# Performance work log

Measured on AMD Instinct MI355X. Metric: run time of the kernel, lower is better.

Reference implementation:

```python
import jax, jax.numpy as jnp
import numpy as np
from jax import lax

N = 100000   # input points
M = 100000   # output points
CIN = 64
COUT = 64
K = 3        # cubic kernel size
G = 50       # grid side (points live at voxel centers of a G^3 grid)
SHIFT = 1    # coordinate shift so border queries (coord -1) stay non-negative
B = 64       # per-axis encode base, > G + K; key fits easily in int32


def _encode(c):
    # c: [..., 3] int32 xyz voxel coords -> unique int32 key
    c = c + SHIFT
    return (c[..., 2] * B + c[..., 1]) * B + c[..., 0]


def setup_inputs() -> dict:
    rng = np.random.RandomState(0)
    total = G ** 3

    def decode(idx):
        x = idx % G
        y = (idx // G) % G
        z = idx // (G * G)
        # +0.5 moves points to voxel centers (as in the layer's docstring example)
        return np.stack([x, y, z], axis=1).astype(np.float32) + 0.5

    inp_positions = jnp.asarray(decode(rng.permutation(total)[:N]))
    out_positions = jnp.asarray(decode(rng.permutation(total)[:M]))

    key = jax.random.key(0)
    k1, k2 = jax.random.split(key, 2)
    inp_features = jax.random.normal(k1, (N, CIN), jnp.float32)
    kernel = jax.random.normal(k2, (K, K, K, CIN, COUT), jnp.float32) * 0.05
    bias = jnp.zeros((COUT,), jnp.float32)
    voxel_size = jnp.ones((), jnp.float32)
    return {
        "inp_features": inp_features,
        "inp_positions": inp_positions,
        "out_positions": out_positions,
        "voxel_size": voxel_size,
        "kernel": kernel,
        "bias": bias,
    }


def reference(inp_features, inp_positions, out_positions, voxel_size, kernel, bias):
    # SparseConv on a regular grid: odd cubic kernel -> offset = 0, Linf radius
    # K*voxel*0.51 selects exactly the K^3 voxel neighborhood. Nearest-neighbor
    # interpolation with identity mapping maps relative offset d in [-r, r]^3
    # to filter tap index d + r on each axis (x = width = last spatial dim).
    inp_coord = jnp.floor(inp_positions / voxel_size).astype(jnp.int32)  # [N,3]
    out_coord = jnp.floor(out_positions / voxel_size).astype(jnp.int32)  # [M,3]

    # sorted-key hash table over input voxels
    keys = _encode(inp_coord)                    # [N]
    order = jnp.argsort(keys)
    skeys = keys[order]
    feats = inp_features[order]                  # [N, Cin]

    r = K // 2
    K3 = K ** 3
    ks = jnp.arange(K3)
    # flat kernel order is (z, y, x) to match kernel.reshape(K3, Cin, Cout)
    d_xyz = jnp.stack([ks % K - r, (ks // K) % K - r, ks // (K * K) - r],
                      axis=1).astype(jnp.int32)  # [K3, 3]
    Kmat = kernel.reshape(K3, CIN, COUT)

    n_inp = skeys.shape[0]

    def step(acc, xs):
        d, W = xs                                 # d: [3], W: [Cin, Cout]
        qk = _encode(out_coord + d)               # [M]
        p = jnp.searchsorted(skeys, qk)
        pc = jnp.clip(p, 0, n_inp - 1)
        found = (skeys[pc] == qk)[:, None]        # [M, 1]
        g = jnp.where(found, feats[pc], 0.0)      # [M, Cin]
        return acc + g @ W, None

    out0 = jnp.zeros((out_coord.shape[0], COUT), inp_features.dtype)
    out, _ = lax.scan(step, out0, (d_xyz, Kmat))
    return out + bias
```

## Files before the change

### kernel.cpp

```cpp
#include <hip/hip_runtime.h>
#include <math.h>

#define GY 54
#define ZD 58
#define NROWS (ZD*GY*64)

#define HX 10
#define HY 6
#define HXY 60
#define NH 600
#define NBX 7
#define NBY 13
#define NBZ 7
#define NBRICK (NBX*NBY*NBZ)
#define SLAB 80

#define TAPS_C0 14
#define TAPS_C1 13

typedef __bf16  bf16x8 __attribute__((ext_vector_type(8)));
typedef float  f32x16 __attribute__((ext_vector_type(16)));

__global__ void prep_kernel(const float* __restrict__ ipos, int n,
                            const float* __restrict__ opos, int m,
                            const float* __restrict__ vsp,
                            const float* __restrict__ W,
                            int* __restrict__ imap, int* __restrict__ ikey,
                            int* __restrict__ omap, int* __restrict__ okey,
                            __bf16* __restrict__ Wt4) {
    int i = blockIdx.x * 256 + threadIdx.x;
    float vs = vsp[0];
    if (i < n) {
        int x = (int)floorf(ipos[3*i+0] / vs) + 1;
        int y = (int)floorf(ipos[3*i+1] / vs) + 1;
        int z = (int)floorf(ipos[3*i+2] / vs) + 1;
        int key = (z * GY + y) * 64 + x;
        ikey[i] = key;
        imap[key] = i;
    } else if (i < n + m) {
        int j = i - n;
        int x = (int)floorf(opos[3*j+0] / vs) + 1;
        int y = (int)floorf(opos[3*j+1] / vs) + 1;
        int z = (int)floorf(opos[3*j+2] / vs) + 1;
        int key = (z * GY + y) * 64 + x;
        okey[j] = key;
        omap[key] = j;
    } else if (i < n + m + 27*64*64) {
        int k  = i - n - m;
        int t  = k >> 12;
        int r  = k & 4095;
        int ci = r >> 6;
        int co = r & 63;
        int p   = ci >> 4;
        int cil = ci & 15;
        Wt4[(((p * 27 + t) << 6) + co) * 16 + cil] = (__bf16)W[k];
    }
}

#define TAP_BODY(t, tc)                                                       \
    {                                                                         \
        const int dx = (t) % 3 - 1;                                           \
        const int dy = ((t) / 3) % 3 - 1;                                     \
        const int dz = (t) / 9 - 1;                                           \
        const int doff = (dz * HXY + dy * HX + dx) * 16;                      \
        bf16x8 a0 = *(const bf16x8*)(Ab0 + doff);                             \
        bf16x8 a1 = *(const bf16x8*)(Ab1 + doff);                             \
        bf16x8 b0 = *(const bf16x8*)(Bb0 + (tc) * 1024);                      \
        bf16x8 b1 = *(const bf16x8*)(Bb1 + (tc) * 1024);                      \
        acc00 = __builtin_amdgcn_mfma_f32_32x32x16_bf16(a0, b0, acc00, 0, 0, 0); \
        acc01 = __builtin_amdgcn_mfma_f32_32x32x16_bf16(a0, b1, acc01, 0, 0, 0); \
        acc10 = __builtin_amdgcn_mfma_f32_32x32x16_bf16(a1, b0, acc10, 0, 0, 0); \
        acc11 = __builtin_amdgcn_mfma_f32_32x32x16_bf16(a1, b1, acc11, 0, 0, 0); \
    }

__global__ __launch_bounds__(256, 2) void conv_kernel(
    const float* __restrict__ feats,
    const __bf16* __restrict__ Wt4,
    const float* __restrict__ bias,
    const int*   __restrict__ imap,
    const int*   __restrict__ ikey,
    const int*   __restrict__ omap,
    const int*   __restrict__ okey,
    float*       __restrict__ out,
    int N, int M)
{
    __shared__ __align__(16) __bf16 halo[NH * 16];
    __shared__ __align__(16) __bf16 Bq[TAPS_C0 * 64 * 16];
    __shared__ int ridx[NH];
    __shared__ int obuf[256];

    const int tid = threadIdx.x;

    int q = (blockIdx.x & 7) * SLAB + (blockIdx.x >> 3);
    if (q >= NBRICK) return;
    const int bx = q % NBX;
    int rem = q / NBX;
    const int by = rem % NBY;
    const int bz = rem / NBY;

    #pragma unroll
    for (int it = 0; it < 3; ++it) {
        int r = it * 256 + tid;
        if (r < NH) {
            int xs = r % HX;
            int t2 = r / HX;
            int ys = t2 % HY;
            int zs = t2 / HY;
            int key = ((bz*8 + zs) * GY + (by*4 + ys)) * 64 + (bx*8 + xs);
            int idx = imap[key];
            int c = min(max(idx, 0), N - 1);
            ridx[r] = (idx >= 0 && idx < N && ikey[c] == key) ? idx : -1;
        }
    }
    {
        int x = tid & 7, y = (tid >> 3) & 3, z = tid >> 5;
        int key = ((bz*8 + z + 1) * GY + (by*4 + y + 1)) * 64 + (bx*8 + x + 1);
        int o = omap[key];
        int c = min(max(o, 0), M - 1);
        obuf[tid] = (o >= 0 && o < M && okey[c] == key) ? o : -1;
    }

    const int wave  = tid >> 6;
    const int lane  = tid & 63;
    const int lrow  = lane & 31;
    const int halfk = lane >> 5;
    const int xv = lrow & 7, yv = (lrow >> 3) & 3;
    const int arow0 = (2*wave + 1) * HXY + (yv + 1) * HX + (xv + 1);
    const __bf16* Ab0 = halo + arow0 * 16 + halfk * 8;
    const __bf16* Ab1 = Ab0 + HXY * 16;
    const __bf16* Bb0 = Bq + lrow * 16 + halfk * 8;
    const __bf16* Bb1 = Bb0 + 32 * 16;

    f32x16 acc00, acc01, acc10, acc11;
    #pragma unroll
    for (int i = 0; i < 16; ++i) { acc00[i]=0.f; acc01[i]=0.f; acc10[i]=0.f; acc11[i]=0.f; }

    __syncthreads();

    #pragma unroll 1
    for (int p = 0; p < 4; ++p) {
        if (p) __syncthreads();

        #pragma unroll
        for (int it = 0; it < 5; ++it) {
            int task = it * 256 + tid;
            if (task < NH * 2) {
                int r = task >> 1, hf = task & 1;
                int idx = ridx[r];
                bf16x8 v;
                if (idx >= 0) {
                    const float4* s = (const float4*)(feats + (size_t)idx * 64 + p * 16 + hf * 8);
                    float4 f0 = s[0], f1 = s[1];
                    v[0]=(__bf16)f0.x; v[1]=(__bf16)f0.y; v[2]=(__bf16)f0.z; v[3]=(__bf16)f0.w;
                    v[4]=(__bf16)f1.x; v[5]=(__bf16)f1.y; v[6]=(__bf16)f1.z; v[7]=(__bf16)f1.w;
                } else {
                    #pragma unroll
                    for (int j = 0; j < 8; ++j) v[j] = (__bf16)0.f;
                }
                *(bf16x8*)(halo + r * 16 + hf * 8) = v;
            }
        }

        {
            const __bf16* Wp = Wt4 + (size_t)p * 27648;
            #pragma unroll
            for (int it = 0; it < 7; ++it) {
                int task = it * 256 + tid;
                *(bf16x8*)(Bq + task * 8) = *(const bf16x8*)(Wp + task * 8);
            }
        }

        __syncthreads();

        #pragma unroll
        for (int t = 0; t < TAPS_C0; ++t) TAP_BODY(t, t)

        __syncthreads();

        {
            const __bf16* Wp = Wt4 + (size_t)p * 27648 + TAPS_C0 * 1024;
            #pragma unroll
            for (int it = 0; it < 7; ++it) {
                int task = it * 256 + tid;
                if (task < TAPS_C1 * 128)
                    *(bf16x8*)(Bq + task * 8) = *(const bf16x8*)(Wp + task * 8);
            }
        }

        __syncthreads();

        #pragma unroll
        for (int t = TAPS_C0; t < 27; ++t) TAP_BODY(t, t - TAPS_C0)
    }

    const int col0 = lrow, col1 = 32 + lrow;
    const float bv0 = bias[col0], bv1 = bias[col1];
    #pragma unroll
    for (int r = 0; r < 16; ++r) {
        int mrow = (r & 3) + 8 * (r >> 2) + 4 * halfk;
        int o0 = obuf[(2*wave)     * 32 + mrow];
        int o1 = obuf[(2*wave + 1) * 32 + mrow];
        if (o0 >= 0) {
            out[(size_t)o0 * 64 + col0] = acc00[r] + bv0;
            out[(size_t)o0 * 64 + col1] = acc01[r] + bv1;
        }
        if (o1 >= 0) {
            out[(size_t)o1 * 64 + col0] = acc10[r] + bv0;
            out[(size_t)o1 * 64 + col1] = acc11[r] + bv1;
        }
    }
}

extern "C" void kernel_launch(void* const* d_in, const int* in_sizes, int n_in,
                              void* d_out, int out_size, void* d_ws, size_t ws_size,
                              hipStream_t stream) {
    const float* feats = (const float*)d_in[0];
    const float* ipos  = (const float*)d_in[1];
    const float* opos  = (const float*)d_in[2];
    const float* vsp   = (const float*)d_in[3];
    const float* W     = (const float*)d_in[4];
    const float* bias  = (const float*)d_in[5];

    int N = in_sizes[0] / 64;
    int M = out_size / 64;

    int*    imap = (int*)d_ws;
    int*    omap = imap + NROWS;
    int*    ikey = omap + NROWS;
    int*    okey = ikey + N;
    __bf16* Wt4  = (__bf16*)(okey + M);

    int total = N + M + 27*64*64;
    prep_kernel<<<(total + 255) / 256, 256, 0, stream>>>(ipos, N, opos, M, vsp, W,
                                                         imap, ikey, omap, okey, Wt4);
    conv_kernel<<<8 * SLAB, 256, 0, stream>>>(feats, Wt4, bias, imap, ikey, omap, okey,
                                              (float*)d_out, N, M);
}
```

Measured before the change: 164.3 us.

## Pre-convert features to bf16 and load halo/weights via direct global-to-LDS loads

The prep kernel now converts the input features to a bf16 copy and writes a small zero row. The conv kernel then fills the halo and weight tiles with global_load_lds instead of staging them through registers, using the zero row for empty voxels. The halo halves are XOR-swizzled so MFMA operand reads avoid LDS bank conflicts, and launch bounds go from 2 to 3 blocks per CU. The cost is an extra full pass over the features in the prep kernel plus more workspace, in exchange for lower register pressure and fewer load and convert instructions in the main kernel.

```diff
diff --git a/kernel.cpp b/kernel.cpp
--- a/kernel.cpp
+++ b/kernel.cpp
@@ -18,16 +18,26 @@
 #define TAPS_C0 14
 #define TAPS_C1 13
 
+#define K3CC (27*64*64)
+
 typedef __bf16  bf16x8 __attribute__((ext_vector_type(8)));
 typedef float  f32x16 __attribute__((ext_vector_type(16)));
+
+#define AS1 __attribute__((address_space(1)))
+#define AS3 __attribute__((address_space(3)))
+#define GLD_LDS16(g, l) \
+    __builtin_amdgcn_global_load_lds((const AS1 void*)(g), (AS3 void*)(l), 16, 0, 0)
 
 __global__ void prep_kernel(const float* __restrict__ ipos, int n,
                             const float* __restrict__ opos, int m,
                             const float* __restrict__ vsp,
                             const float* __restrict__ W,
+                            const float* __restrict__ feats,
                             int* __restrict__ imap, int* __restrict__ ikey,
                             int* __restrict__ omap, int* __restrict__ okey,
-                            __bf16* __restrict__ Wt4) {
+                            __bf16* __restrict__ Wt4,
+                            __bf16* __restrict__ zrow,
+                            __bf16* __restrict__ featsB) {
     int i = blockIdx.x * 256 + threadIdx.x;
     float vs = vsp[0];
     if (i < n) {
@@ -45,7 +55,7 @@
         int key = (z * GY + y) * 64 + x;
         okey[j] = key;
         omap[key] = j;
-    } else if (i < n + m + 27*64*64) {
+    } else if (i < n + m + K3CC) {
         int k  = i - n - m;
         int t  = k >> 12;
         int r  = k & 4095;
@@ -54,28 +64,43 @@
         int p   = ci >> 4;
         int cil = ci & 15;
         Wt4[(((p * 27 + t) << 6) + co) * 16 + cil] = (__bf16)W[k];
+    } else if (i < n + m + K3CC + 32) {
+        zrow[i - n - m - K3CC] = (__bf16)0.f;
+    } else {
+        int j = i - n - m - K3CC - 32;
+        if (j < n * 8) {
+            const float4* s = (const float4*)(feats + (size_t)j * 8);
+            float4 f0 = s[0], f1 = s[1];
+            bf16x8 v;
+            v[0]=(__bf16)f0.x; v[1]=(__bf16)f0.y; v[2]=(__bf16)f0.z; v[3]=(__bf16)f0.w;
+            v[4]=(__bf16)f1.x; v[5]=(__bf16)f1.y; v[6]=(__bf16)f1.z; v[7]=(__bf16)f1.w;
+            *(bf16x8*)(featsB + (size_t)j * 8) = v;
+        }
     }
 }
 
-#define TAP_BODY(t, tc)                                                       \
-    {                                                                         \
-        const int dx = (t) % 3 - 1;                                           \
-        const int dy = ((t) / 3) % 3 - 1;                                     \
-        const int dz = (t) / 9 - 1;                                           \
-        const int doff = (dz * HXY + dy * HX + dx) * 16;                      \
-        bf16x8 a0 = *(const bf16x8*)(Ab0 + doff);                             \
-        bf16x8 a1 = *(const bf16x8*)(Ab1 + doff);                             \
-        bf16x8 b0 = *(const bf16x8*)(Bb0 + (tc) * 1024);                      \
-        bf16x8 b1 = *(const bf16x8*)(Bb1 + (tc) * 1024);                      \
+#define TAP_BODY(t, tc)                                                        \
+    {                                                                          \
+        const int drow = ((t)/9 - 1)*HXY + (((t)/3)%3 - 1)*HX + ((t)%3 - 1);   \
+        int rb  = abase + drow * 32;                                           \
+        int ad0 = rb + (((rb >> 3) & 16) ^ hk16);                              \
+        int rb1 = rb + HXY * 32;                                               \
+        int ad1 = rb1 + (((rb1 >> 3) & 16) ^ hk16);                            \
+        bf16x8 a0 = *(const bf16x8*)(haloc + ad0);                             \
+        bf16x8 a1 = *(const bf16x8*)(haloc + ad1);                             \
+        bf16x8 b0 = *(const bf16x8*)(Bb0 + (tc) * 1024);                       \
+        bf16x8 b1 = *(const bf16x8*)(Bb1 + (tc) * 1024);                       \
         acc00 = __builtin_amdgcn_mfma_f32_32x32x16_bf16(a0, b0, acc00, 0, 0, 0); \
         acc01 = __builtin_amdgcn_mfma_f32_32x32x16_bf16(a0, b1, acc01, 0, 0, 0); \
         acc10 = __builtin_amdgcn_mfma_f32_32x32x16_bf16(a1, b0, acc10, 0, 0, 0); \
         acc11 = __builtin_amdgcn_mfma_f32_32x32x16_bf16(a1, b1, acc11, 0, 0, 0); \
     }
 
-__global__ __launch_bounds__(256, 2) void conv_kernel(
+__global__ __launch_bounds__(256, 3) void conv_kernel(
     const float* __restrict__ feats,
+    const __bf16* __restrict__ featsB,
     const __bf16* __restrict__ Wt4,
+    const __bf16* __restrict__ zrow,
     const float* __restrict__ bias,
     const int*   __restrict__ imap,
     const int*   __restrict__ ikey,
@@ -126,8 +151,9 @@
     const int halfk = lane >> 5;
     const int xv = lrow & 7, yv = (lrow >> 3) & 3;
     const int arow0 = (2*wave + 1) * HXY + (yv + 1) * HX + (xv + 1);
-    const __bf16* Ab0 = halo + arow0 * 16 + halfk * 8;
-    const __bf16* Ab1 = Ab0 + HXY * 16;
+    const int abase = arow0 * 32;
+    const int hk16  = halfk * 16;
+    const char* haloc = (const char*)halo;
     const __bf16* Bb0 = Bq + lrow * 16 + halfk * 8;
     const __bf16* Bb1 = Bb0 + 32 * 16;
 
@@ -145,19 +171,13 @@
         for (int it = 0; it < 5; ++it) {
             int task = it * 256 + tid;
             if (task < NH * 2) {
-                int r = task >> 1, hf = task & 1;
+                int r  = task >> 1;
+                int hl = (task & 1) ^ ((r >> 2) & 1);
                 int idx = ridx[r];
-                bf16x8 v;
-                if (idx >= 0) {
-                    const float4* s = (const float4*)(feats + (size_t)idx * 64 + p * 16 + hf * 8);
-                    float4 f0 = s[0], f1 = s[1];
-                    v[0]=(__bf16)f0.x; v[1]=(__bf16)f0.y; v[2]=(__bf16)f0.z; v[3]=(__bf16)f0.w;
-                    v[4]=(__bf16)f1.x; v[5]=(__bf16)f1.y; v[6]=(__bf16)f1.z; v[7]=(__bf16)f1.w;
-                } else {
-                    #pragma unroll
-                    for (int j = 0; j < 8; ++j) v[j] = (__bf16)0.f;
-                }
-                *(bf16x8*)(halo + r * 16 + hf * 8) = v;
+                const __bf16* src = (idx >= 0)
+                    ? featsB + (size_t)idx * 64 + p * 16 + hl * 8
+                    : zrow;
+                GLD_LDS16(src, (char*)halo + task * 16);
             }
         }
 
@@ -166,7 +186,7 @@
             #pragma unroll
             for (int it = 0; it < 7; ++it) {
                 int task = it * 256 + tid;
-                *(bf16x8*)(Bq + task * 8) = *(const bf16x8*)(Wp + task * 8);
+                GLD_LDS16(Wp + task * 8, (char*)Bq + task * 16);
             }
         }
 
@@ -183,7 +203,7 @@
             for (int it = 0; it < 7; ++it) {
                 int task = it * 256 + tid;
                 if (task < TAPS_C1 * 128)
-                    *(bf16x8*)(Bq + task * 8) = *(const bf16x8*)(Wp + task * 8);
+                    GLD_LDS16(Wp + task * 8, (char*)Bq + task * 16);
             }
         }
 
@@ -224,15 +244,19 @@
     int N = in_sizes[0] / 64;
     int M = out_size / 64;
 
-    int*    imap = (int*)d_ws;
-    int*    omap = imap + NROWS;
-    int*    ikey = omap + NROWS;
-    int*    okey = ikey + N;
-    __bf16* Wt4  = (__bf16*)(okey + M);
-
-    int total = N + M + 27*64*64;
-    prep_kernel<<<(total + 255) / 256, 256, 0, stream>>>(ipos, N, opos, M, vsp, W,
-                                                         imap, ikey, omap, okey, Wt4);
-    conv_kernel<<<8 * SLAB, 256, 0, stream>>>(feats, Wt4, bias, imap, ikey, omap, okey,
+    int*    imap   = (int*)d_ws;
+    int*    omap   = imap + NROWS;
+    int*    ikey   = omap + NROWS;
+    int*    okey   = ikey + N;
+    __bf16* Wt4    = (__bf16*)(okey + M);
+    __bf16* zrow   = Wt4 + K3CC;
+    __bf16* featsB = zrow + 32;
+
+    int total = N + M + K3CC + 32 + N * 8;
+    prep_kernel<<<(total + 255) / 256, 256, 0, stream>>>(ipos, N, opos, M, vsp, W, feats,
+                                                         imap, ikey, omap, okey,
+                                                         Wt4, zrow, featsB);
+    conv_kernel<<<8 * SLAB, 256, 0, stream>>>(feats, featsB, Wt4, zrow, bias,
+                                              imap, ikey, omap, okey,
                                               (float*)d_out, N, M);
 }
```

After: 206.3 us. 1.26x slower.
